# Optimization experiments

Hardware: AMD Instinct MI355X
Metric: run time of the kernel (lower is better)

## Reference

```python
import jax, jax.numpy as jnp
import numpy as np

CO, NO, ITERATIONS, STRIDE = 32, 8, 3, 2


def _squash(x, axis):
    norm = jnp.linalg.norm(x, axis=axis, keepdims=True)
    return x * norm / (1.0 + norm ** 2)


def _quantize(x, bits):
    # Faithful instantiation: identity quantization (full-precision pass-through),
    # matching running the original module with quantization_function = lambda t, b: t.
    return x


def setup_inputs() -> dict:
    key = jax.random.key(0)
    k1, k2, k3 = jax.random.split(key, 3)
    x = jax.random.normal(k1, (16, 256, 1, 20, 20), dtype=jnp.float32)
    W = jax.random.normal(k2, (CO * NO, 1, 9, 9), dtype=jnp.float32) * 0.05  # Conv2d weight [co*no, ni, k, k]
    bias = jax.random.normal(k3, (CO, NO, 1, 1), dtype=jnp.float32) * 0.01
    return {"x": x, "W": W, "bias": bias,
            "quantization_bits": 8, "quantization_bits_routing": 8}


def reference(x, W, bias, quantization_bits, quantization_bits_routing):
    bs, ci, ni, hi, wi = x.shape
    # vote generation: conv over each input capsule channel independently
    lhs = x.reshape(bs * ci, ni, hi, wi)
    votes = jax.lax.conv_general_dilated(
        lhs, W, window_strides=(STRIDE, STRIDE), padding='VALID',
        dimension_numbers=('NCHW', 'OIHW', 'NCHW'))
    votes = _quantize(votes, quantization_bits)
    ho, wo = votes.shape[-2:]
    votes = votes.reshape(bs, ci, CO, NO, ho, wo)  # [bs, ci, co, no, ho, wo]

    logits = jnp.zeros((bs, ci, CO, ho, wo), dtype=votes.dtype)
    activation = None
    for _ in range(ITERATIONS):
        route = jax.nn.softmax(logits, axis=2)                      # c_ij over co
        route = _quantize(route, quantization_bits)
        # s_j = sum_i c_ij * u_hat_{j|i} + bias  -> [bs, co, no, ho, wo]
        preactivate = jnp.einsum('bichw,bicnhw->bcnhw', route, votes) + bias
        preactivate = _quantize(preactivate, quantization_bits_routing)
        activation = _squash(preactivate, axis=2)                   # squash over no
        activation = _quantize(activation, quantization_bits)
        # agreement: <u_hat_{j|i}, v_j> summed over no -> [bs, ci, co, ho, wo]
        distances = jnp.einsum('bicnhw,bcnhw->bichw', votes, activation)
        logits = _quantize(logits + distances, quantization_bits_routing)
    return activation
```

## Files before the change

### kernel.cpp

```cpp
#include <hip/hip_runtime.h>


#define BS 16
#define CI 256
#define CO 32
#define NO 8
#define HI 20
#define WI 20
#define HO 6
#define WO 6
#define NPIX 36
#define NTAP 81
#define XP 104
#define NBLK 576

typedef __attribute__((ext_vector_type(8))) short bf16x8;
typedef __attribute__((ext_vector_type(4))) float f32x4;

__device__ __forceinline__ ushort f2bf(float x) {
    union { float f; unsigned u; } v; v.f = x;
    unsigned r = v.u + 0x7FFFu + ((v.u >> 16) & 1u);
    return (ushort)(r >> 16);
}

template<int CTRL>
__device__ __forceinline__ float dpp_radd(float v) {
    int s = __builtin_amdgcn_update_dpp(0, __float_as_int(v), CTRL, 0xF, 0xF, true);
    return v + __int_as_float(s);
}
__device__ __forceinline__ float row16_sum_tail(float v) {
    v = dpp_radd<0x111>(v);
    v = dpp_radd<0x112>(v);
    v = dpp_radd<0x114>(v);
    v = dpp_radd<0x118>(v);
    return v;
}
__device__ __forceinline__ float grp8_sum_all(float v) {
    v = dpp_radd<0xB1>(v);
    v = dpp_radd<0x4E>(v);
    v = dpp_radd<0x141>(v);
    return v;
}

__global__ __launch_bounds__(1024) void caps_kernel(
    const float* __restrict__ x,
    const float* __restrict__ Wt,
    const float* __restrict__ bias,
    float* __restrict__ out)
{
    __shared__ __align__(16) ushort xw[CI * XP];
    __shared__ __align__(16) ushort wl[CO * NO * XP];
    __shared__ __align__(16) float  smx[4 * 256];
    __shared__ __align__(16) float  pre[4 * 256];
    __shared__ __align__(16) float  act[256];

    const int t   = threadIdx.x, blk = blockIdx.x;
    const int b   = blk & 15;
    const int hw  = blk >> 4;
    const int h   = hw / WO, w = hw % WO;
    const int w2  = 2 * w;

    const int wid = t >> 6, l = t & 63;
    const int q = l >> 4, il = l & 15;
    const int wf = wid >> 2, wi = wid & 3;

    for (int p = t; p < CO * NO * NTAP; p += 1024) {
        int f = p / NTAP, k = p - f * NTAP;
        wl[f * XP + k] = f2bf(Wt[p]);
    }
    {
        int i = t >> 2, s4 = t & 3;
        #pragma unroll
        for (int j = 0; j < 6; ++j) {
            int k = NTAP + s4 * 6 + j;
            if (k < XP) { xw[i * XP + k] = 0; wl[i * XP + k] = 0; }
        }
    }
    #pragma unroll
    for (int pass = 0; pass < 9; ++pass) {
        int idx = pass * 1024 + t;
        int q4 = idx & 3, r = idx >> 2;
        int kh = r % 9, i = r / 9;
        float4 v = *(const float4*)(x + ((b * CI + i) * HI + (2 * h + kh)) * WI + 4 * q4);
        const float* ve = &v.x;
        #pragma unroll
        for (int e = 0; e < 4; ++e) {
            int kw = 4 * q4 + e - w2;
            if ((unsigned)kw < 9u) xw[i * XP + kh * 9 + kw] = f2bf(ve[e]);
        }
    }
    if (w >= 4) {
        for (int r = t; r < CI * 9; r += 1024) {
            int kh = r % 9, i = r / 9;
            float4 v = *(const float4*)(x + ((b * CI + i) * HI + (2 * h + kh)) * WI + 16);
            const float* ve = &v.x;
            #pragma unroll
            for (int e = 0; e < 4; ++e) {
                int kw = 16 + e - w2;
                if ((unsigned)kw < 9u) xw[i * XP + kh * 9 + kw] = f2bf(ve[e]);
            }
        }
    }

    const float bias_r = (t < 256) ? bias[t] : 0.f;
    __syncthreads();

    f32x4 acc[4][4];
    #pragma unroll
    for (int tf = 0; tf < 4; ++tf)
        #pragma unroll
        for (int ti = 0; ti < 4; ++ti)
            acc[tf][ti] = (f32x4){0.f, 0.f, 0.f, 0.f};

    #pragma unroll
    for (int ks = 0; ks < 3; ++ks) {
        const int ko = ks * 32 + q * 8;
        bf16x8 af[4], bv[4];
        #pragma unroll
        for (int tf = 0; tf < 4; ++tf)
            af[tf] = *(const bf16x8*)&wl[(wf * 64 + tf * 16 + il) * XP + ko];
        #pragma unroll
        for (int ti = 0; ti < 4; ++ti)
            bv[ti] = *(const bf16x8*)&xw[(wi * 64 + ti * 16 + il) * XP + ko];
        #pragma unroll
        for (int tf = 0; tf < 4; ++tf)
            #pragma unroll
            for (int ti = 0; ti < 4; ++ti)
                acc[tf][ti] = __builtin_amdgcn_mfma_f32_16x16x32_bf16(
                    af[tf], bv[ti], acc[tf][ti], 0, 0, 0);
    }

    float lg[4][4];
    #pragma unroll
    for (int tf = 0; tf < 4; ++tf)
        #pragma unroll
        for (int ti = 0; ti < 4; ++ti) lg[tf][ti] = 0.f;

    #pragma unroll
    for (int it = 0; it < 3; ++it) {
        float pp[4][4];
        if (it == 0) {
            #pragma unroll
            for (int tf = 0; tf < 4; ++tf)
                #pragma unroll
                for (int r = 0; r < 4; ++r)
                    pp[tf][r] = (acc[tf][0][r] + acc[tf][1][r]
                               + acc[tf][2][r] + acc[tf][3][r]) * 0.03125f;
        } else {
            float e[4][4], srow[4] = {0.f, 0.f, 0.f, 0.f};
            #pragma unroll
            for (int tf = 0; tf < 4; ++tf)
                #pragma unroll
                for (int ti = 0; ti < 4; ++ti) {
                    e[tf][ti] = __expf(lg[tf][ti]);
                    srow[ti] += e[tf][ti];
                }
            #pragma unroll
            for (int ti = 0; ti < 4; ++ti)
                srow[ti] += __shfl_xor(srow[ti], 32, 64);
            if (q == 0) {
                #pragma unroll
                for (int ti = 0; ti < 4; ++ti)
                    smx[wf * 256 + wi * 64 + ti * 16 + il] = srow[ti];
            }
            __syncthreads();
            float rtot[4];
            #pragma unroll
            for (int ti = 0; ti < 4; ++ti) {
                int i = wi * 64 + ti * 16 + il;
                rtot[ti] = __builtin_amdgcn_rcpf(
                    smx[i] + smx[256 + i] + smx[512 + i] + smx[768 + i]);
            }
            float route[4][4];
            #pragma unroll
            for (int tf = 0; tf < 4; ++tf)
                #pragma unroll
                for (int ti = 0; ti < 4; ++ti) route[tf][ti] = e[tf][ti] * rtot[ti];
            #pragma unroll
            for (int tf = 0; tf < 4; ++tf)
                #pragma unroll
                for (int r = 0; r < 4; ++r)
                    pp[tf][r] = route[tf][0] * acc[tf][0][r] + route[tf][1] * acc[tf][1][r]
                              + route[tf][2] * acc[tf][2][r] + route[tf][3] * acc[tf][3][r];
        }

        #pragma unroll
        for (int tf = 0; tf < 4; ++tf)
            #pragma unroll
            for (int r = 0; r < 4; ++r)
                pp[tf][r] = row16_sum_tail(pp[tf][r]);
        if (il == 15) {
            #pragma unroll
            for (int tf = 0; tf < 4; ++tf) {
                int c = wf * 8 + tf * 2 + (q >> 1);
                f32x4 vv = {pp[tf][0], pp[tf][1], pp[tf][2], pp[tf][3]};
                *(f32x4*)&pre[wi * 256 + c * 8 + (q & 1) * 4] = vv;
            }
        }
        __syncthreads();

        if (t < 256) {
            float s = bias_r + pre[t] + pre[256 + t] + pre[512 + t] + pre[768 + t];
            float sq = grp8_sum_all(s * s);
            float a = s * __builtin_amdgcn_sqrtf(sq) * __builtin_amdgcn_rcpf(1.f + sq);
            if (it == 2) {
                int c = t >> 3, n = t & 7;
                out[(((b * CO + c) * NO + n) * HO + h) * WO + w] = a;
            } else {
                act[t] = a;
            }
        }

        if (it < 2) {
            __syncthreads();
            #pragma unroll
            for (int tf = 0; tf < 4; ++tf) {
                int c = wf * 8 + tf * 2 + (q >> 1);
                f32x4 av = *(const f32x4*)&act[c * 8 + (q & 1) * 4];
                #pragma unroll
                for (int ti = 0; ti < 4; ++ti) {
                    float d = acc[tf][ti][0] * av[0] + acc[tf][ti][1] * av[1]
                            + acc[tf][ti][2] * av[2] + acc[tf][ti][3] * av[3];
                    d += __shfl_xor(d, 16, 64);
                    lg[tf][ti] += d;
                }
            }
        }
    }
}

extern "C" void kernel_launch(void* const* d_in, const int* in_sizes, int n_in,
                              void* d_out, int out_size, void* d_ws, size_t ws_size,
                              hipStream_t stream) {
    const float* x    = (const float*)d_in[0];
    const float* Wt   = (const float*)d_in[1];
    const float* bias = (const float*)d_in[2];
    float* out = (float*)d_out;
    caps_kernel<<<NBLK, 1024, 0, stream>>>(x, Wt, bias, out);
}
```

Baseline: 48.32 us.

## Compute squash redundantly per wave to drop a barrier and use permlane swaps

Every wave now reads the four partial pre-activation slices plus bias from shared memory and computes the squash for its own capsule rows itself. This removes the separate 256-thread squash phase, the act buffer and one block-wide barrier per routing iteration. Cross-lane reductions by 16 and 32 lanes use permlane16/32 swap builtins when they are available instead of ds_swizzle/bpermute shuffles. The cost is redundant squash arithmetic and extra shared-memory reads across all waves.

```diff
diff --git a/kernel.cpp b/kernel.cpp
--- a/kernel.cpp
+++ b/kernel.cpp
@@ -35,12 +35,24 @@
     v = dpp_radd<0x118>(v);
     return v;
 }
-__device__ __forceinline__ float grp8_sum_all(float v) {
-    v = dpp_radd<0xB1>(v);
-    v = dpp_radd<0x4E>(v);
-    v = dpp_radd<0x141>(v);
-    return v;
-}
+#if __has_builtin(__builtin_amdgcn_permlane16_swap)
+typedef unsigned u32x2 __attribute__((ext_vector_type(2)));
+__device__ __forceinline__ float xor16_sum(float v) {
+    u32x2 r = __builtin_amdgcn_permlane16_swap(__float_as_uint(v), __float_as_uint(v), false, false);
+    return __uint_as_float(r.x) + __uint_as_float(r.y);
+}
+#else
+__device__ __forceinline__ float xor16_sum(float v) { return v + __shfl_xor(v, 16, 64); }
+#endif
+#if __has_builtin(__builtin_amdgcn_permlane32_swap)
+typedef unsigned u32x2b __attribute__((ext_vector_type(2)));
+__device__ __forceinline__ float xor32_sum(float v) {
+    u32x2b r = __builtin_amdgcn_permlane32_swap(__float_as_uint(v), __float_as_uint(v), false, false);
+    return __uint_as_float(r.x) + __uint_as_float(r.y);
+}
+#else
+__device__ __forceinline__ float xor32_sum(float v) { return v + __shfl_xor(v, 32, 64); }
+#endif
 
 __global__ __launch_bounds__(1024) void caps_kernel(
     const float* __restrict__ x,
@@ -52,7 +64,7 @@
     __shared__ __align__(16) ushort wl[CO * NO * XP];
     __shared__ __align__(16) float  smx[4 * 256];
     __shared__ __align__(16) float  pre[4 * 256];
-    __shared__ __align__(16) float  act[256];
+    __shared__ __align__(16) float  bb[256];
 
     const int t   = threadIdx.x, blk = blockIdx.x;
     const int b   = blk & 15;
@@ -68,6 +80,7 @@
         int f = p / NTAP, k = p - f * NTAP;
         wl[f * XP + k] = f2bf(Wt[p]);
     }
+    if (t < 256) bb[t] = bias[t];
     {
         int i = t >> 2, s4 = t & 3;
         #pragma unroll
@@ -102,7 +115,6 @@
         }
     }
 
-    const float bias_r = (t < 256) ? bias[t] : 0.f;
     __syncthreads();
 
     f32x4 acc[4][4];
@@ -157,7 +169,7 @@
                 }
             #pragma unroll
             for (int ti = 0; ti < 4; ++ti)
-                srow[ti] += __shfl_xor(srow[ti], 32, 64);
+                srow[ti] = xor32_sum(srow[ti]);
             if (q == 0) {
                 #pragma unroll
                 for (int ti = 0; ti < 4; ++ti)
@@ -199,31 +211,36 @@
         }
         __syncthreads();
 
-        if (t < 256) {
-            float s = bias_r + pre[t] + pre[256 + t] + pre[512 + t] + pre[768 + t];
-            float sq = grp8_sum_all(s * s);
-            float a = s * __builtin_amdgcn_sqrtf(sq) * __builtin_amdgcn_rcpf(1.f + sq);
-            if (it == 2) {
-                int c = t >> 3, n = t & 7;
-                out[(((b * CO + c) * NO + n) * HO + h) * WO + w] = a;
-            } else {
-                act[t] = a;
-            }
-        }
-
-        if (it < 2) {
-            __syncthreads();
-            #pragma unroll
-            for (int tf = 0; tf < 4; ++tf) {
-                int c = wf * 8 + tf * 2 + (q >> 1);
-                f32x4 av = *(const f32x4*)&act[c * 8 + (q & 1) * 4];
+        #pragma unroll
+        for (int tf = 0; tf < 4; ++tf) {
+            const int c8 = (wf * 8 + tf * 2 + (q >> 1)) * 8 + (q & 1) * 4;
+            f32x4 p0 = *(const f32x4*)&pre[c8];
+            f32x4 p1 = *(const f32x4*)&pre[256 + c8];
+            f32x4 p2 = *(const f32x4*)&pre[512 + c8];
+            f32x4 p3 = *(const f32x4*)&pre[768 + c8];
+            f32x4 bv4 = *(const f32x4*)&bb[c8];
+            float s[4], sq4 = 0.f;
+            #pragma unroll
+            for (int r = 0; r < 4; ++r) {
+                s[r] = bv4[r] + p0[r] + p1[r] + p2[r] + p3[r];
+                sq4 += s[r] * s[r];
+            }
+            float sq = xor16_sum(sq4);
+            float scale = __builtin_amdgcn_sqrtf(sq) * __builtin_amdgcn_rcpf(1.f + sq);
+            if (it < 2) {
                 #pragma unroll
                 for (int ti = 0; ti < 4; ++ti) {
-                    float d = acc[tf][ti][0] * av[0] + acc[tf][ti][1] * av[1]
-                            + acc[tf][ti][2] * av[2] + acc[tf][ti][3] * av[3];
-                    d += __shfl_xor(d, 16, 64);
-                    lg[tf][ti] += d;
+                    float d = acc[tf][ti][0] * (s[0] * scale)
+                            + acc[tf][ti][1] * (s[1] * scale)
+                            + acc[tf][ti][2] * (s[2] * scale)
+                            + acc[tf][ti][3] * (s[3] * scale);
+                    lg[tf][ti] += xor16_sum(d);
                 }
+            } else if (wi == 0 && il == 0) {
+                const int c = wf * 8 + tf * 2 + (q >> 1);
+                #pragma unroll
+                for (int r = 0; r < 4; ++r)
+                    out[((b * CO + c) * NO + (4 * (q & 1) + r)) * NPIX + hw] = s[r] * scale;
             }
         }
     }
```

Result: slower. 74.45 us (+54.1%).

## Make blocks persistent over multiple pixels, overlap next x staging with routing

Applied to the files above, without the earlier changes.

Cuts the grid from 576 to 256 blocks. Each block now handles two or three output pixels, so the bf16 weight tile in LDS is converted and staged once and reused across pixels. Staging the next pixel's input patch into LDS is placed before the current pixel's routing iterations so the two can overlap. Cross-lane reductions now use permlane swap builtins where available. The risks are fewer blocks than CUs, with uneven load (3 vs 2 pixels) lengthening the tail, and extra barriers per pixel.

```diff
diff --git a/kernel.cpp b/kernel.cpp
--- a/kernel.cpp
+++ b/kernel.cpp
@@ -12,7 +12,7 @@
 #define NPIX 36
 #define NTAP 81
 #define XP 104
-#define NBLK 576
+#define NBLK 256
 
 typedef __attribute__((ext_vector_type(8))) short bf16x8;
 typedef __attribute__((ext_vector_type(4))) float f32x4;
@@ -40,6 +40,55 @@
     v = dpp_radd<0x4E>(v);
     v = dpp_radd<0x141>(v);
     return v;
+}
+#if __has_builtin(__builtin_amdgcn_permlane16_swap)
+typedef unsigned u32x2 __attribute__((ext_vector_type(2)));
+__device__ __forceinline__ float xor16_sum(float v) {
+    u32x2 r = __builtin_amdgcn_permlane16_swap(__float_as_uint(v), __float_as_uint(v), false, false);
+    return __uint_as_float(r.x) + __uint_as_float(r.y);
+}
+#else
+__device__ __forceinline__ float xor16_sum(float v) { return v + __shfl_xor(v, 16, 64); }
+#endif
+#if __has_builtin(__builtin_amdgcn_permlane32_swap)
+typedef unsigned u32x2b __attribute__((ext_vector_type(2)));
+__device__ __forceinline__ float xor32_sum(float v) {
+    u32x2b r = __builtin_amdgcn_permlane32_swap(__float_as_uint(v), __float_as_uint(v), false, false);
+    return __uint_as_float(r.x) + __uint_as_float(r.y);
+}
+#else
+__device__ __forceinline__ float xor32_sum(float v) { return v + __shfl_xor(v, 32, 64); }
+#endif
+
+__device__ __forceinline__ void stage_x(const float* __restrict__ xb,
+                                        ushort* __restrict__ xw,
+                                        int t, int h, int w) {
+    const int w2 = 2 * w;
+    #pragma unroll
+    for (int pass = 0; pass < 9; ++pass) {
+        int idx = pass * 1024 + t;
+        int q4 = idx & 3, r = idx >> 2;
+        int kh = r % 9, i = r / 9;
+        float4 v = *(const float4*)(xb + (i * HI + 2 * h + kh) * WI + 4 * q4);
+        const float* ve = &v.x;
+        #pragma unroll
+        for (int e = 0; e < 4; ++e) {
+            int kw = 4 * q4 + e - w2;
+            if ((unsigned)kw < 9u) xw[i * XP + kh * 9 + kw] = f2bf(ve[e]);
+        }
+    }
+    if (w >= 4) {
+        for (int r = t; r < CI * 9; r += 1024) {
+            int kh = r % 9, i = r / 9;
+            float4 v = *(const float4*)(xb + (i * HI + 2 * h + kh) * WI + 16);
+            const float* ve = &v.x;
+            #pragma unroll
+            for (int e = 0; e < 4; ++e) {
+                int kw = 16 + e - w2;
+                if ((unsigned)kw < 9u) xw[i * XP + kh * 9 + kw] = f2bf(ve[e]);
+            }
+        }
+    }
 }
 
 __global__ __launch_bounds__(1024) void caps_kernel(
@@ -56,9 +105,8 @@
 
     const int t   = threadIdx.x, blk = blockIdx.x;
     const int b   = blk & 15;
-    const int hw  = blk >> 4;
-    const int h   = hw / WO, w = hw % WO;
-    const int w2  = 2 * w;
+    const int npix = (blk < 64) ? 3 : 2;
+    const float* xb = x + b * CI * HI * WI;
 
     const int wid = t >> 6, l = t & 63;
     const int q = l >> 4, il = l & 15;
@@ -76,153 +124,141 @@
             if (k < XP) { xw[i * XP + k] = 0; wl[i * XP + k] = 0; }
         }
     }
-    #pragma unroll
-    for (int pass = 0; pass < 9; ++pass) {
-        int idx = pass * 1024 + t;
-        int q4 = idx & 3, r = idx >> 2;
-        int kh = r % 9, i = r / 9;
-        float4 v = *(const float4*)(x + ((b * CI + i) * HI + (2 * h + kh)) * WI + 4 * q4);
-        const float* ve = &v.x;
-        #pragma unroll
-        for (int e = 0; e < 4; ++e) {
-            int kw = 4 * q4 + e - w2;
-            if ((unsigned)kw < 9u) xw[i * XP + kh * 9 + kw] = f2bf(ve[e]);
-        }
-    }
-    if (w >= 4) {
-        for (int r = t; r < CI * 9; r += 1024) {
-            int kh = r % 9, i = r / 9;
-            float4 v = *(const float4*)(x + ((b * CI + i) * HI + (2 * h + kh)) * WI + 16);
-            const float* ve = &v.x;
-            #pragma unroll
-            for (int e = 0; e < 4; ++e) {
-                int kw = 16 + e - w2;
-                if ((unsigned)kw < 9u) xw[i * XP + kh * 9 + kw] = f2bf(ve[e]);
-            }
-        }
-    }
+    stage_x(xb, xw, t, (blk >> 4) / WO, (blk >> 4) % WO);
 
     const float bias_r = (t < 256) ? bias[t] : 0.f;
-    __syncthreads();
-
-    f32x4 acc[4][4];
-    #pragma unroll
-    for (int tf = 0; tf < 4; ++tf)
-        #pragma unroll
-        for (int ti = 0; ti < 4; ++ti)
-            acc[tf][ti] = (f32x4){0.f, 0.f, 0.f, 0.f};
-
-    #pragma unroll
-    for (int ks = 0; ks < 3; ++ks) {
-        const int ko = ks * 32 + q * 8;
-        bf16x8 af[4], bv[4];
+
+    for (int p = 0; p < npix; ++p) {
+        const int hw = (blk + 256 * p) >> 4;
+        const int h  = hw / WO, w = hw % WO;
+
+        __syncthreads();
+
+        f32x4 acc[4][4];
         #pragma unroll
         for (int tf = 0; tf < 4; ++tf)
-            af[tf] = *(const bf16x8*)&wl[(wf * 64 + tf * 16 + il) * XP + ko];
-        #pragma unroll
-        for (int ti = 0; ti < 4; ++ti)
-            bv[ti] = *(const bf16x8*)&xw[(wi * 64 + ti * 16 + il) * XP + ko];
+            #pragma unroll
+            for (int ti = 0; ti < 4; ++ti)
+                acc[tf][ti] = (f32x4){0.f, 0.f, 0.f, 0.f};
+
+        #pragma unroll
+        for (int ks = 0; ks < 3; ++ks) {
+            const int ko = ks * 32 + q * 8;
+            bf16x8 af[4], bv[4];
+            #pragma unroll
+            for (int tf = 0; tf < 4; ++tf)
+                af[tf] = *(const bf16x8*)&wl[(wf * 64 + tf * 16 + il) * XP + ko];
+            #pragma unroll
+            for (int ti = 0; ti < 4; ++ti)
+                bv[ti] = *(const bf16x8*)&xw[(wi * 64 + ti * 16 + il) * XP + ko];
+            #pragma unroll
+            for (int tf = 0; tf < 4; ++tf)
+                #pragma unroll
+                for (int ti = 0; ti < 4; ++ti)
+                    acc[tf][ti] = __builtin_amdgcn_mfma_f32_16x16x32_bf16(
+                        af[tf], bv[ti], acc[tf][ti], 0, 0, 0);
+        }
+
+        __syncthreads();
+
+        if (p + 1 < npix) {
+            const int hwn = (blk + 256 * (p + 1)) >> 4;
+            stage_x(xb, xw, t, hwn / WO, hwn % WO);
+        }
+
+        float lg[4][4];
         #pragma unroll
         for (int tf = 0; tf < 4; ++tf)
             #pragma unroll
-            for (int ti = 0; ti < 4; ++ti)
-                acc[tf][ti] = __builtin_amdgcn_mfma_f32_16x16x32_bf16(
-                    af[tf], bv[ti], acc[tf][ti], 0, 0, 0);
-    }
-
-    float lg[4][4];
-    #pragma unroll
-    for (int tf = 0; tf < 4; ++tf)
-        #pragma unroll
-        for (int ti = 0; ti < 4; ++ti) lg[tf][ti] = 0.f;
-
-    #pragma unroll
-    for (int it = 0; it < 3; ++it) {
-        float pp[4][4];
-        if (it == 0) {
+            for (int ti = 0; ti < 4; ++ti) lg[tf][ti] = 0.f;
+
+        #pragma unroll
+        for (int it = 0; it < 3; ++it) {
+            float pp[4][4];
+            if (it == 0) {
+                #pragma unroll
+                for (int tf = 0; tf < 4; ++tf)
+                    #pragma unroll
+                    for (int r = 0; r < 4; ++r)
+                        pp[tf][r] = (acc[tf][0][r] + acc[tf][1][r]
+                                   + acc[tf][2][r] + acc[tf][3][r]) * 0.03125f;
+            } else {
+                float e[4][4], srow[4] = {0.f, 0.f, 0.f, 0.f};
+                #pragma unroll
+                for (int tf = 0; tf < 4; ++tf)
+                    #pragma unroll
+                    for (int ti = 0; ti < 4; ++ti) {
+                        e[tf][ti] = __expf(lg[tf][ti]);
+                        srow[ti] += e[tf][ti];
+                    }
+                #pragma unroll
+                for (int ti = 0; ti < 4; ++ti)
+                    srow[ti] = xor32_sum(srow[ti]);
+                if (q == 0) {
+                    #pragma unroll
+                    for (int ti = 0; ti < 4; ++ti)
+                        smx[wf * 256 + wi * 64 + ti * 16 + il] = srow[ti];
+                }
+                __syncthreads();
+                float rtot[4];
+                #pragma unroll
+                for (int ti = 0; ti < 4; ++ti) {
+                    int i = wi * 64 + ti * 16 + il;
+                    rtot[ti] = __builtin_amdgcn_rcpf(
+                        smx[i] + smx[256 + i] + smx[512 + i] + smx[768 + i]);
+                }
+                float route[4][4];
+                #pragma unroll
+                for (int tf = 0; tf < 4; ++tf)
+                    #pragma unroll
+                    for (int ti = 0; ti < 4; ++ti) route[tf][ti] = e[tf][ti] * rtot[ti];
+                #pragma unroll
+                for (int tf = 0; tf < 4; ++tf)
+                    #pragma unroll
+                    for (int r = 0; r < 4; ++r)
+                        pp[tf][r] = route[tf][0] * acc[tf][0][r] + route[tf][1] * acc[tf][1][r]
+                                  + route[tf][2] * acc[tf][2][r] + route[tf][3] * acc[tf][3][r];
+            }
+
             #pragma unroll
             for (int tf = 0; tf < 4; ++tf)
                 #pragma unroll
                 for (int r = 0; r < 4; ++r)
-                    pp[tf][r] = (acc[tf][0][r] + acc[tf][1][r]
-                               + acc[tf][2][r] + acc[tf][3][r]) * 0.03125f;
-        } else {
-            float e[4][4], srow[4] = {0.f, 0.f, 0.f, 0.f};
-            #pragma unroll
-            for (int tf = 0; tf < 4; ++tf)
-                #pragma unroll
-                for (int ti = 0; ti < 4; ++ti) {
-                    e[tf][ti] = __expf(lg[tf][ti]);
-                    srow[ti] += e[tf][ti];
-                }
-            #pragma unroll
-            for (int ti = 0; ti < 4; ++ti)
-                srow[ti] += __shfl_xor(srow[ti], 32, 64);
-            if (q == 0) {
-                #pragma unroll
-                for (int ti = 0; ti < 4; ++ti)
-                    smx[wf * 256 + wi * 64 + ti * 16 + il] = srow[ti];
+                    pp[tf][r] = row16_sum_tail(pp[tf][r]);
+            if (il == 15) {
+                #pragma unroll
+                for (int tf = 0; tf < 4; ++tf) {
+                    int c = wf * 8 + tf * 2 + (q >> 1);
+                    f32x4 vv = {pp[tf][0], pp[tf][1], pp[tf][2], pp[tf][3]};
+                    *(f32x4*)&pre[wi * 256 + c * 8 + (q & 1) * 4] = vv;
+                }
             }
             __syncthreads();
-            float rtot[4];
-            #pragma unroll
-            for (int ti = 0; ti < 4; ++ti) {
-                int i = wi * 64 + ti * 16 + il;
-                rtot[ti] = __builtin_amdgcn_rcpf(
-                    smx[i] + smx[256 + i] + smx[512 + i] + smx[768 + i]);
-            }
-            float route[4][4];
-            #pragma unroll
-            for (int tf = 0; tf < 4; ++tf)
-                #pragma unroll
-                for (int ti = 0; ti < 4; ++ti) route[tf][ti] = e[tf][ti] * rtot[ti];
-            #pragma unroll
-            for (int tf = 0; tf < 4; ++tf)
-                #pragma unroll
-                for (int r = 0; r < 4; ++r)
-                    pp[tf][r] = route[tf][0] * acc[tf][0][r] + route[tf][1] * acc[tf][1][r]
-                              + route[tf][2] * acc[tf][2][r] + route[tf][3] * acc[tf][3][r];
-        }
-
-        #pragma unroll
-        for (int tf = 0; tf < 4; ++tf)
-            #pragma unroll
-            for (int r = 0; r < 4; ++r)
-                pp[tf][r] = row16_sum_tail(pp[tf][r]);
-        if (il == 15) {
-            #pragma unroll
-            for (int tf = 0; tf < 4; ++tf) {
-                int c = wf * 8 + tf * 2 + (q >> 1);
-                f32x4 vv = {pp[tf][0], pp[tf][1], pp[tf][2], pp[tf][3]};
-                *(f32x4*)&pre[wi * 256 + c * 8 + (q & 1) * 4] = vv;
-            }
-        }
-        __syncthreads();
-
-        if (t < 256) {
-            float s = bias_r + pre[t] + pre[256 + t] + pre[512 + t] + pre[768 + t];
-            float sq = grp8_sum_all(s * s);
-            float a = s * __builtin_amdgcn_sqrtf(sq) * __builtin_amdgcn_rcpf(1.f + sq);
-            if (it == 2) {
-                int c = t >> 3, n = t & 7;
-                out[(((b * CO + c) * NO + n) * HO + h) * WO + w] = a;
-            } else {
-                act[t] = a;
-            }
-        }
-
-        if (it < 2) {
-            __syncthreads();
-            #pragma unroll
-            for (int tf = 0; tf < 4; ++tf) {
-                int c = wf * 8 + tf * 2 + (q >> 1);
-                f32x4 av = *(const f32x4*)&act[c * 8 + (q & 1) * 4];
-                #pragma unroll
-                for (int ti = 0; ti < 4; ++ti) {
-                    float d = acc[tf][ti][0] * av[0] + acc[tf][ti][1] * av[1]
-                            + acc[tf][ti][2] * av[2] + acc[tf][ti][3] * av[3];
-                    d += __shfl_xor(d, 16, 64);
-                    lg[tf][ti] += d;
+
+            if (t < 256) {
+                float s = bias_r + pre[t] + pre[256 + t] + pre[512 + t] + pre[768 + t];
+                float sq = grp8_sum_all(s * s);
+                float a = s * __builtin_amdgcn_sqrtf(sq) * __builtin_amdgcn_rcpf(1.f + sq);
+                if (it == 2) {
+                    int c = t >> 3, n = t & 7;
+                    out[(((b * CO + c) * NO + n) * HO + h) * WO + w] = a;
+                } else {
+                    act[t] = a;
+                }
+            }
+
+            if (it < 2) {
+                __syncthreads();
+                #pragma unroll
+                for (int tf = 0; tf < 4; ++tf) {
+                    int c = wf * 8 + tf * 2 + (q >> 1);
+                    f32x4 av = *(const f32x4*)&act[c * 8 + (q & 1) * 4];
+                    #pragma unroll
+                    for (int ti = 0; ti < 4; ++ti) {
+                        float d = acc[tf][ti][0] * av[0] + acc[tf][ti][1] * av[1]
+                                + acc[tf][ti][2] * av[2] + acc[tf][ti][3] * av[3];
+                        lg[tf][ti] += xor16_sum(d);
+                    }
                 }
             }
         }
```

Result: slower. 57.20 us (+18.4%).
